# Kernel optimization log

Hardware: AMD Instinct MI355X
Metric: run time of the kernel (lower is better)

## Reference

```python
import jax, jax.numpy as jnp
import numpy as np


def ternary_quantize(t, threshold, scale):
    # values in {-scale, 0, +scale}
    return jnp.where(t > threshold, scale, jnp.where(t < -threshold, -scale, 0.0)).astype(t.dtype)


def setup_inputs() -> dict:
    key = jax.random.key(0)
    k1, k2, k3 = jax.random.split(key, 3)
    B, S, D = 4, 4096, 2048  # batch, seq, d_model (in=out=D)
    x = jax.random.normal(k1, (B, S, D), dtype=jnp.float32)
    weight = jax.random.normal(k2, (D, D), dtype=jnp.float32) * 0.02
    # layer_name == 'query' -> gaussian RRAM variation (std chosen as 0.05, mean 0)
    rram_variation = jax.random.normal(k3, (D, D), dtype=jnp.float32) * 0.05
    return {"x": x, "weight": weight, "rram_variation": rram_variation}


def reference(x, weight, rram_variation):
    TH_X, SC_X = 0.33, 0.5      # activation ternary threshold/scale
    TH_W, SC_W = 0.2, 0.6       # weight ternary threshold (th_value) / scale (clamp_value)
    x_q = ternary_quantize(x, TH_X, SC_X)                 # [B,S,D]
    w_q = ternary_quantize(weight, TH_W, SC_W)            # [O,D]
    w_rram = w_q + rram_variation                         # [O,D]
    # F.linear: x_q @ w_rram.T, no bias
    return jnp.einsum('bsd,od->bso', x_q, w_rram)
```

## Files before the change

kernel.cpp:

```cpp
#include <hip/hip_runtime.h>
#include <hip/hip_bf16.h>
#include <cmath>
#include <cstdint>


#define AS1 __attribute__((address_space(1)))
#define AS3 __attribute__((address_space(3)))

typedef unsigned short u16;
typedef __bf16 bf16x8 __attribute__((ext_vector_type(8)));
typedef float f32x4 __attribute__((ext_vector_type(4)));
typedef unsigned short u16x4 __attribute__((ext_vector_type(4)));

#define BM 128
#define BN 128
#define BK 64

__device__ __forceinline__ u16 f2bf_rne(float f) {
  uint32_t u = __float_as_uint(f);
  u += 0x7FFFu + ((u >> 16) & 1u);
  return (u16)(u >> 16);
}

__device__ __forceinline__ u16 ter_x(float v) {
  double d = (double)v;
  return d > 0.33 ? (u16)0x3F00u : (d < -0.33 ? (u16)0xBF00u : (u16)0u);
}

__device__ __forceinline__ float ter_w(float v) {
  double d = (double)v;
  return d > 0.2 ? 0.6f : (d < -0.2 ? -0.6f : 0.0f);
}

__global__ void quant_x_kernel(const float* __restrict__ x, u16* __restrict__ xq,
                               long n4) {
  long i = (long)blockIdx.x * blockDim.x + threadIdx.x;
  if (i >= n4) return;
  float4 v = ((const float4*)x)[i];
  u16x4 q;
  q.x = ter_x(v.x); q.y = ter_x(v.y); q.z = ter_x(v.z); q.w = ter_x(v.w);
  ((u16x4*)xq)[i] = q;
}

__global__ void quant_w_kernel(const float* __restrict__ w,
                               const float* __restrict__ rr,
                               u16* __restrict__ wq, long n4) {
  long i = (long)blockIdx.x * blockDim.x + threadIdx.x;
  if (i >= n4) return;
  float4 a = ((const float4*)w)[i];
  float4 b = ((const float4*)rr)[i];
  u16x4 q;
  q.x = f2bf_rne(ter_w(a.x) + b.x);
  q.y = f2bf_rne(ter_w(a.y) + b.y);
  q.z = f2bf_rne(ter_w(a.z) + b.z);
  q.w = f2bf_rne(ter_w(a.w) + b.w);
  ((u16x4*)wq)[i] = q;
}

__device__ __forceinline__ void gld_lds16(const void* g, void* l) {
  __builtin_amdgcn_global_load_lds((AS1 void*)g, (AS3 void*)l, 16, 0, 0);
}

template <bool FUSED>
__global__ __launch_bounds__(256) void gemm_bt_kernel(
    const u16* __restrict__ Aq, const float* __restrict__ Xf,
    const u16* __restrict__ Bq, float* __restrict__ C,
    int M, int N, int K) {
  __shared__ u16 As[BM * BK];
  __shared__ u16 Bs[BN * BK];

  const int tid  = threadIdx.x;
  const int wid  = tid >> 6;
  const int lane = tid & 63;

  const int m0 = blockIdx.y * BM;
  const int n0 = blockIdx.x * BN;

  const int r8 = lane >> 3;
  const int c8 = (lane & 7) * 8;

  const int mw = (wid >> 1) * 64;
  const int nw = (wid & 1) * 64;
  const int fr = lane & 15;
  const int fk = (lane >> 4) * 8;

  f32x4 acc[4][4] = {};

  for (int k0 = 0; k0 < K; k0 += BK) {
#pragma unroll
    for (int t = 0; t < 4; ++t) {
      const int rbase = wid * 32 + t * 8;
      gld_lds16(Bq + (size_t)(n0 + rbase + r8) * K + k0 + c8, &Bs[rbase * BK]);
    }
    if constexpr (!FUSED) {
#pragma unroll
      for (int t = 0; t < 4; ++t) {
        const int rbase = wid * 32 + t * 8;
        gld_lds16(Aq + (size_t)(m0 + rbase + r8) * K + k0 + c8, &As[rbase * BK]);
      }
    } else {
#pragma unroll
      for (int it = 0; it < 8; ++it) {
        const int idx = it * 256 + tid;
        const int row = idx >> 4;
        const int c4  = (idx & 15) * 4;
        const float4 v = *(const float4*)&Xf[(size_t)(m0 + row) * K + k0 + c4];
        u16x4 q;
        q.x = ter_x(v.x); q.y = ter_x(v.y); q.z = ter_x(v.z); q.w = ter_x(v.w);
        *(u16x4*)&As[row * BK + c4] = q;
      }
    }
    __syncthreads();

#pragma unroll
    for (int kk = 0; kk < BK; kk += 32) {
      bf16x8 a[4], b[4];
#pragma unroll
      for (int i = 0; i < 4; ++i)
        a[i] = *(const bf16x8*)&As[(mw + i * 16 + fr) * BK + kk + fk];
#pragma unroll
      for (int j = 0; j < 4; ++j)
        b[j] = *(const bf16x8*)&Bs[(nw + j * 16 + fr) * BK + kk + fk];
#pragma unroll
      for (int i = 0; i < 4; ++i)
#pragma unroll
        for (int j = 0; j < 4; ++j)
          acc[i][j] =
              __builtin_amdgcn_mfma_f32_16x16x32_bf16(a[i], b[j], acc[i][j], 0, 0, 0);
    }
    __syncthreads();
  }

  const int om = m0 + mw + (lane >> 4) * 4;
  const int on = n0 + nw + (lane & 15);
#pragma unroll
  for (int i = 0; i < 4; ++i)
#pragma unroll
    for (int j = 0; j < 4; ++j)
#pragma unroll
      for (int r = 0; r < 4; ++r)
        C[(size_t)(om + i * 16 + r) * N + (on + j * 16)] = acc[i][j][r];
}

extern "C" void kernel_launch(void* const* d_in, const int* in_sizes, int n_in,
                              void* d_out, int out_size, void* d_ws, size_t ws_size,
                              hipStream_t stream) {
  const float* x  = (const float*)d_in[0];
  const float* w  = (const float*)d_in[1];
  const float* rr = (const float*)d_in[2];
  float* out = (float*)d_out;

  const long xn = (long)in_sizes[0];
  const long wn = (long)in_sizes[1];
  const int K = (int)llround(std::sqrt((double)wn));
  const int N = K;
  const int M = (int)(xn / K);

  u16* wq = (u16*)d_ws;
  u16* xq = (u16*)d_ws + (size_t)N * K;
  const size_t need = ((size_t)M * K + (size_t)N * K) * sizeof(u16);

  {
    long n4 = wn / 4;
    quant_w_kernel<<<(int)((n4 + 255) / 256), 256, 0, stream>>>(w, rr, wq, n4);
  }

  dim3 grid(N / BN, M / BM);
  if (ws_size >= need) {
    long n4 = xn / 4;
    quant_x_kernel<<<(int)((n4 + 255) / 256), 256, 0, stream>>>(x, xq, n4);
    gemm_bt_kernel<false><<<grid, 256, 0, stream>>>(xq, nullptr, wq, out, M, N, K);
  } else {
    gemm_bt_kernel<true><<<grid, 256, 0, stream>>>(nullptr, x, wq, out, M, N, K);
  }
}
```

Baseline: 421.4 us.

## Use 256x256 tile GEMM with 4-stage async LDS pipeline and swizzled layout

Replaces the 128x128 single-buffered GEMM with a 512-thread 256x256 tile kernel that uses BK=32 and four LDS buffers. Tiles are prefetched three steps ahead with global_load_lds and waited on with explicit vmcnt counts, so global loads overlap MFMA work. The LDS layout is XOR-swizzled to cut bank conflicts, and s_setprio raises priority around the MFMA block. The cost is 128KB of LDS per block, which limits occupancy to one block per CU, and more accumulator registers per thread.

```diff
diff --git a/kernel.cpp b/kernel.cpp
--- a/kernel.cpp
+++ b/kernel.cpp
@@ -12,9 +12,10 @@
 typedef float f32x4 __attribute__((ext_vector_type(4)));
 typedef unsigned short u16x4 __attribute__((ext_vector_type(4)));
 
-#define BM 128
-#define BN 128
-#define BK 64
+#define BM 256
+#define BN 256
+#define BK 32
+#define NBUF 4
 
 __device__ __forceinline__ u16 f2bf_rne(float f) {
   uint32_t u = __float_as_uint(f);
@@ -61,24 +62,107 @@
   __builtin_amdgcn_global_load_lds((AS1 void*)g, (AS3 void*)l, 16, 0, 0);
 }
 
-template <bool FUSED>
-__global__ __launch_bounds__(256) void gemm_bt_kernel(
-    const u16* __restrict__ Aq, const float* __restrict__ Xf,
-    const u16* __restrict__ Bq, float* __restrict__ C,
-    int M, int N, int K) {
-  __shared__ u16 As[BM * BK];
-  __shared__ u16 Bs[BN * BK];
+__global__ __launch_bounds__(512, 2) void gemm256_kernel(
+    const u16* __restrict__ Aq, const u16* __restrict__ Bq,
+    float* __restrict__ C, int M, int N, int K) {
+  __shared__ u16 lds[NBUF * 16384];
 
   const int tid  = threadIdx.x;
   const int wid  = tid >> 6;
   const int lane = tid & 63;
+  const int wm = wid >> 2;
+  const int wn = wid & 3;
 
   const int m0 = blockIdx.y * BM;
   const int n0 = blockIdx.x * BN;
 
+  const int srow = wid * 16 + (lane >> 2);
+  const int scol = ((lane & 3) * 8) ^ ((lane & 32) ? 16 : 0);
+  const u16* pa = Aq + (size_t)(m0 + srow) * K + scol;
+  const u16* pb = Bq + (size_t)(n0 + srow) * K + scol;
+  const size_t slot1 = (size_t)128 * K;
+  const int sd = wid * 512;
+
+  const int fr  = lane & 15;
+  const int fk  = (lane >> 4) * 8;
+  const int col = fk ^ ((fr & 8) ? 16 : 0);
+  const int aoff = (wm * 128 + fr) * 32 + col;
+  const int boff = 8192 + (wn * 64 + fr) * 32 + col;
+
+  f32x4 acc[8][4] = {};
+  const int nt = K / BK;
+
+#pragma unroll
+  for (int T = 0; T < 3; ++T) {
+    const int bb = T * 16384;
+    const u16* at = pa + (size_t)T * BK;
+    const u16* bt = pb + (size_t)T * BK;
+    gld_lds16(at,         &lds[bb + sd]);
+    gld_lds16(at + slot1, &lds[bb + sd + 4096]);
+    gld_lds16(bt,         &lds[bb + 8192 + sd]);
+    gld_lds16(bt + slot1, &lds[bb + 8192 + sd + 4096]);
+  }
+
+  for (int t = 0; t < nt; ++t) {
+    if (t < nt - 2)       asm volatile("s_waitcnt vmcnt(8)" ::: "memory");
+    else if (t == nt - 2) asm volatile("s_waitcnt vmcnt(4)" ::: "memory");
+    else                  asm volatile("s_waitcnt vmcnt(0)" ::: "memory");
+    __builtin_amdgcn_sched_barrier(0);
+    __builtin_amdgcn_s_barrier();
+    __builtin_amdgcn_sched_barrier(0);
+
+    const int Tn = t + 3;
+    if (Tn < nt) {
+      const int bb = (Tn & 3) * 16384;
+      const u16* at = pa + (size_t)Tn * BK;
+      const u16* bt = pb + (size_t)Tn * BK;
+      gld_lds16(at,         &lds[bb + sd]);
+      gld_lds16(at + slot1, &lds[bb + sd + 4096]);
+      gld_lds16(bt,         &lds[bb + 8192 + sd]);
+      gld_lds16(bt + slot1, &lds[bb + 8192 + sd + 4096]);
+    }
+
+    const int rb = (t & 3) * 16384;
+    bf16x8 a[8], b[4];
+#pragma unroll
+    for (int i = 0; i < 8; ++i) a[i] = *(const bf16x8*)&lds[rb + aoff + i * 512];
+#pragma unroll
+    for (int j = 0; j < 4; ++j) b[j] = *(const bf16x8*)&lds[rb + boff + j * 512];
+
+    __builtin_amdgcn_s_setprio(1);
+#pragma unroll
+    for (int i = 0; i < 8; ++i)
+#pragma unroll
+      for (int j = 0; j < 4; ++j)
+        acc[i][j] =
+            __builtin_amdgcn_mfma_f32_16x16x32_bf16(a[i], b[j], acc[i][j], 0, 0, 0);
+    __builtin_amdgcn_s_setprio(0);
+  }
+
+  const int om = m0 + wm * 128 + (lane >> 4) * 4;
+  const int on = n0 + wn * 64 + (lane & 15);
+#pragma unroll
+  for (int i = 0; i < 8; ++i)
+#pragma unroll
+    for (int j = 0; j < 4; ++j)
+#pragma unroll
+      for (int r = 0; r < 4; ++r)
+        C[(size_t)(om + i * 16 + r) * N + (on + j * 16)] = acc[i][j][r];
+}
+
+__global__ __launch_bounds__(256) void gemm_fused128_kernel(
+    const float* __restrict__ Xf, const u16* __restrict__ Bq,
+    float* __restrict__ C, int M, int N, int K) {
+  __shared__ u16 As[128 * 64];
+  __shared__ u16 Bs[128 * 64];
+
+  const int tid  = threadIdx.x;
+  const int wid  = tid >> 6;
+  const int lane = tid & 63;
+  const int m0 = blockIdx.y * 128;
+  const int n0 = blockIdx.x * 128;
   const int r8 = lane >> 3;
   const int c8 = (lane & 7) * 8;
-
   const int mw = (wid >> 1) * 64;
   const int nw = (wid & 1) * 64;
   const int fr = lane & 15;
@@ -86,41 +170,33 @@
 
   f32x4 acc[4][4] = {};
 
-  for (int k0 = 0; k0 < K; k0 += BK) {
+  for (int k0 = 0; k0 < K; k0 += 64) {
 #pragma unroll
     for (int t = 0; t < 4; ++t) {
       const int rbase = wid * 32 + t * 8;
-      gld_lds16(Bq + (size_t)(n0 + rbase + r8) * K + k0 + c8, &Bs[rbase * BK]);
-    }
-    if constexpr (!FUSED) {
-#pragma unroll
-      for (int t = 0; t < 4; ++t) {
-        const int rbase = wid * 32 + t * 8;
-        gld_lds16(Aq + (size_t)(m0 + rbase + r8) * K + k0 + c8, &As[rbase * BK]);
-      }
-    } else {
-#pragma unroll
-      for (int it = 0; it < 8; ++it) {
-        const int idx = it * 256 + tid;
-        const int row = idx >> 4;
-        const int c4  = (idx & 15) * 4;
-        const float4 v = *(const float4*)&Xf[(size_t)(m0 + row) * K + k0 + c4];
-        u16x4 q;
-        q.x = ter_x(v.x); q.y = ter_x(v.y); q.z = ter_x(v.z); q.w = ter_x(v.w);
-        *(u16x4*)&As[row * BK + c4] = q;
-      }
+      gld_lds16(Bq + (size_t)(n0 + rbase + r8) * K + k0 + c8, &Bs[rbase * 64]);
+    }
+#pragma unroll
+    for (int it = 0; it < 8; ++it) {
+      const int idx = it * 256 + tid;
+      const int row = idx >> 4;
+      const int c4  = (idx & 15) * 4;
+      const float4 v = *(const float4*)&Xf[(size_t)(m0 + row) * K + k0 + c4];
+      u16x4 q;
+      q.x = ter_x(v.x); q.y = ter_x(v.y); q.z = ter_x(v.z); q.w = ter_x(v.w);
+      *(u16x4*)&As[row * 64 + c4] = q;
     }
     __syncthreads();
 
 #pragma unroll
-    for (int kk = 0; kk < BK; kk += 32) {
+    for (int kk = 0; kk < 64; kk += 32) {
       bf16x8 a[4], b[4];
 #pragma unroll
       for (int i = 0; i < 4; ++i)
-        a[i] = *(const bf16x8*)&As[(mw + i * 16 + fr) * BK + kk + fk];
+        a[i] = *(const bf16x8*)&As[(mw + i * 16 + fr) * 64 + kk + fk];
 #pragma unroll
       for (int j = 0; j < 4; ++j)
-        b[j] = *(const bf16x8*)&Bs[(nw + j * 16 + fr) * BK + kk + fk];
+        b[j] = *(const bf16x8*)&Bs[(nw + j * 16 + fr) * 64 + kk + fk];
 #pragma unroll
       for (int i = 0; i < 4; ++i)
 #pragma unroll
@@ -165,12 +241,15 @@
     quant_w_kernel<<<(int)((n4 + 255) / 256), 256, 0, stream>>>(w, rr, wq, n4);
   }
 
-  dim3 grid(N / BN, M / BM);
-  if (ws_size >= need) {
+  const bool ok256 = (M % BM == 0) && (N % BN == 0) && (K % BK == 0) &&
+                     (K / BK >= 4) && (ws_size >= need);
+  if (ok256) {
     long n4 = xn / 4;
     quant_x_kernel<<<(int)((n4 + 255) / 256), 256, 0, stream>>>(x, xq, n4);
-    gemm_bt_kernel<false><<<grid, 256, 0, stream>>>(xq, nullptr, wq, out, M, N, K);
+    dim3 grid(N / BN, M / BM);
+    gemm256_kernel<<<grid, 512, 0, stream>>>(xq, wq, out, M, N, K);
   } else {
-    gemm_bt_kernel<true><<<grid, 256, 0, stream>>>(nullptr, x, wq, out, M, N, K);
-  }
-}
+    dim3 grid(N / 128, M / 128);
+    gemm_fused128_kernel<<<grid, 256, 0, stream>>>(x, wq, out, M, N, K);
+  }
+}
```

Result: faster. 368.2 us (-12.6%).
